# Optimization experiments

Hardware: AMD Instinct MI355X
Metric: run time of the kernel (lower is better)

The kernel has to match this reference:

```python
import jax, jax.numpy as jnp
import numpy as np

N, F, B = 16384, 1024, 512


def setup_inputs() -> dict:
    key = jax.random.key(0)
    k1, k2, k3, k4, k5 = jax.random.split(key, 5)
    s = 1.0 / np.sqrt(F + B)
    return {
        "behavior": jax.random.normal(k1, (N, B), dtype=jnp.float32),
        "h_prev": jax.random.normal(k2, (N, F), dtype=jnp.float32),
        "c_prev": jax.random.normal(k3, (N, F), dtype=jnp.float32),
        "Wh": jax.random.normal(k4, (4 * F, F), dtype=jnp.float32) * s,
        "Wx": jax.random.normal(k5, (4 * F, B), dtype=jnp.float32) * s,
        "b": jnp.zeros((4 * F,), dtype=jnp.float32),
    }


def reference(behavior, h_prev, c_prev, Wh, Wx, b):
    # Fused single GEMM for all 4 gates: [n, 4F]
    gates = jnp.einsum("nf,gf->ng", h_prev, Wh) + jnp.einsum("nb,gb->ng", behavior, Wx) + b
    i, f, g, o = jnp.split(gates, 4, axis=-1)
    i = jax.nn.sigmoid(i)
    f = jax.nn.sigmoid(f)
    g = jnp.tanh(g)
    o = jax.nn.sigmoid(o)
    c = f * c_prev + i * g
    h = o * jnp.tanh(c)
    return h
```

## Files before the change

kernel.cpp:

```cpp
#include <hip/hip_runtime.h>
#include <hip/hip_bf16.h>
#include <stdint.h>

#define N_ROWS 16384
#define F_DIM  1024
#define B_DIM  512
#define K_DIM  1536
#define G_DIM  4096
#define CB_STR 36

typedef __bf16 v8bf __attribute__((ext_vector_type(8)));
typedef float  v4f  __attribute__((ext_vector_type(4)));

typedef const void __attribute__((address_space(1)))* gptr1;
typedef void       __attribute__((address_space(3)))* lptr3;

__device__ __forceinline__ unsigned short f2bf(float x) {
    union { float f; unsigned int u; } c; c.f = x;
    unsigned int u = c.u;
    return (unsigned short)((u + 0x7FFFu + ((u >> 16) & 1u)) >> 16);
}

__global__ void pack_x(const float* __restrict__ behavior,
                       const float* __restrict__ h_prev,
                       unsigned short* __restrict__ A) {
    const int row = blockIdx.x;
    const int col = threadIdx.x * 8;
    const float* src = (col < F_DIM)
        ? h_prev   + (long)row * F_DIM + col
        : behavior + (long)row * B_DIM + (col - F_DIM);
    float4 lo = *(const float4*)src;
    float4 hi = *(const float4*)(src + 4);
    union { unsigned short u[8]; int4 v; } p;
    p.u[0] = f2bf(lo.x); p.u[1] = f2bf(lo.y); p.u[2] = f2bf(lo.z); p.u[3] = f2bf(lo.w);
    p.u[4] = f2bf(hi.x); p.u[5] = f2bf(hi.y); p.u[6] = f2bf(hi.z); p.u[7] = f2bf(hi.w);
    *(int4*)(A + (long)row * K_DIM + col) = p.v;
}

__global__ void pack_w(const float* __restrict__ Wh,
                       const float* __restrict__ Wx,
                       const float* __restrict__ b,
                       unsigned short* __restrict__ W,
                       float* __restrict__ bperm) {
    const int gp   = blockIdx.x;
    const int gate = gp & 3;
    const int f    = gp >> 2;
    const int g    = gate * F_DIM + f;
    const int col  = threadIdx.x * 8;
    const float* src = (col < F_DIM)
        ? Wh + (long)g * F_DIM + col
        : Wx + (long)g * B_DIM + (col - F_DIM);
    float4 lo = *(const float4*)src;
    float4 hi = *(const float4*)(src + 4);
    union { unsigned short u[8]; int4 v; } p;
    p.u[0] = f2bf(lo.x); p.u[1] = f2bf(lo.y); p.u[2] = f2bf(lo.z); p.u[3] = f2bf(lo.w);
    p.u[4] = f2bf(hi.x); p.u[5] = f2bf(hi.y); p.u[6] = f2bf(hi.z); p.u[7] = f2bf(hi.w);
    *(int4*)(W + (long)gp * K_DIM + col) = p.v;
    if (threadIdx.x == 0) bperm[gp] = b[g];
}

__device__ __forceinline__ float sigmoidf_fast(float x) {
    return 1.f / (1.f + __expf(-x));
}
__device__ __forceinline__ float tanhf_fast(float x) {
    return 1.f - 2.f / (__expf(2.f * x) + 1.f);
}

__global__ __launch_bounds__(256, 2) void lstm_gemm(
    const unsigned short* __restrict__ A,
    const unsigned short* __restrict__ W,
    const float* __restrict__ bperm,
    const float* __restrict__ c_prev,
    float* __restrict__ out)
{
    __shared__ unsigned short lds[16384];

    const int m0   = blockIdx.y * 128;
    const int n0   = blockIdx.x * 128;
    const int tid  = threadIdx.x;
    const int lane = tid & 63;
    const int wave = tid >> 6;
    const int wm   = (wave >> 1) * 64;
    const int wn   = (wave & 1) * 64;
    const int lrow = lane & 15;
    const int quad = lane >> 4;
    const int r7   = lrow & 7;

    v4f acc[4][4] = {};

    const int ls_row = lane >> 3;
    const int ls_blk = (lane & 7) ^ ls_row;
    const unsigned short* a_g = A + (long)(m0 + wave * 32 + ls_row) * K_DIM + ls_blk * 8;
    const unsigned short* w_g = W + (long)(n0 + wave * 32 + ls_row) * K_DIM + ls_blk * 8;
    unsigned short* a_l = &lds[(wave * 32) * 64];
    unsigned short* w_l = &lds[8192 + (wave * 32) * 64];

    for (int k0 = 0; k0 < K_DIM; k0 += 64) {
#pragma unroll
        for (int c = 0; c < 4; ++c) {
            __builtin_amdgcn_global_load_lds((gptr1)(a_g + (long)c * 8 * K_DIM + k0),
                                             (lptr3)(a_l + c * 8 * 64), 16, 0, 0);
            __builtin_amdgcn_global_load_lds((gptr1)(w_g + (long)c * 8 * K_DIM + k0),
                                             (lptr3)(w_l + c * 8 * 64), 16, 0, 0);
        }
        __syncthreads();

#pragma unroll
        for (int kk = 0; kk < 64; kk += 32) {
            const int ko = kk >> 3;
            const int sa = (((quad + ko) ^ r7) * 8);
            v8bf af[4], bf[4];
#pragma unroll
            for (int mt = 0; mt < 4; ++mt)
                af[mt] = *(const v8bf*)&lds[(wm + mt * 16 + lrow) * 64 + sa];
#pragma unroll
            for (int nt = 0; nt < 4; ++nt)
                bf[nt] = *(const v8bf*)&lds[8192 + (wn + nt * 16 + lrow) * 64 + sa];
#pragma unroll
            for (int mt = 0; mt < 4; ++mt)
#pragma unroll
                for (int nt = 0; nt < 4; ++nt)
                    acc[mt][nt] = __builtin_amdgcn_mfma_f32_16x16x32_bf16(
                        af[mt], bf[nt], acc[mt][nt], 0, 0, 0);
        }
        __syncthreads();
    }

    float* cbuf = (float*)lds;
    const int fbase = n0 >> 2;
#pragma unroll
    for (int i = 0; i < 4; ++i) {
        const int q  = i * 256 + tid;
        const int r  = q >> 3;
        const int c4 = (q & 7) * 4;
        *(float4*)&cbuf[r * CB_STR + c4] =
            *(const float4*)&c_prev[(long)(m0 + r) * F_DIM + fbase + c4];
    }
    __syncthreads();

    const int l3 = lane & 3;
    const int fl = (lane & 15) >> 2;
#pragma unroll
    for (int nt = 0; nt < 4; ++nt) {
        const int   gcol = n0 + wn + nt * 16 + lrow;
        const float bias = bperm[gcol];
#pragma unroll
        for (int mt = 0; mt < 4; ++mt) {
            float a0 = acc[mt][nt][0] + bias;
            float a1 = acc[mt][nt][1] + bias;
            float a2 = acc[mt][nt][2] + bias;
            float a3 = acc[mt][nt][3] + bias;
            float s0 = (lane & 1) ? a0 : a1;
            float s1 = (lane & 1) ? a2 : a3;
            float r0 = __shfl_xor(s0, 1, 64);
            float r1 = __shfl_xor(s1, 1, 64);
            if (lane & 1) { a0 = r0; a2 = r1; } else { a1 = r0; a3 = r1; }
            s0 = (lane & 2) ? a0 : a2;
            s1 = (lane & 2) ? a1 : a3;
            r0 = __shfl_xor(s0, 2, 64);
            r1 = __shfl_xor(s1, 2, 64);
            if (lane & 2) { a0 = r0; a1 = r1; } else { a2 = r0; a3 = r1; }
            const float iv = sigmoidf_fast(a0);
            const float fv = sigmoidf_fast(a1);
            const float gv = tanhf_fast(a2);
            const float ov = sigmoidf_fast(a3);
            const int lr = wm + mt * 16 + quad * 4 + l3;
            const int lc = ((wn + nt * 16) >> 2) + fl;
            const float cp = cbuf[lr * CB_STR + lc];
            const float cv = fv * cp + iv * gv;
            cbuf[lr * CB_STR + lc] = ov * tanhf_fast(cv);
        }
    }
    __syncthreads();

#pragma unroll
    for (int i = 0; i < 4; ++i) {
        const int q  = i * 256 + tid;
        const int r  = q >> 3;
        const int c4 = (q & 7) * 4;
        *(float4*)&out[(long)(m0 + r) * F_DIM + fbase + c4] =
            *(const float4*)&cbuf[r * CB_STR + c4];
    }
}

extern "C" void kernel_launch(void* const* d_in, const int* in_sizes, int n_in,
                              void* d_out, int out_size, void* d_ws, size_t ws_size,
                              hipStream_t stream) {
    const float* behavior = (const float*)d_in[0];
    const float* h_prev   = (const float*)d_in[1];
    const float* c_prev   = (const float*)d_in[2];
    const float* Wh       = (const float*)d_in[3];
    const float* Wx       = (const float*)d_in[4];
    const float* b        = (const float*)d_in[5];
    float* out = (float*)d_out;

    unsigned short* A  = (unsigned short*)d_ws;
    unsigned short* W  = A + (size_t)N_ROWS * K_DIM;
    float*       bperm = (float*)(W + (size_t)G_DIM * K_DIM);

    pack_x<<<N_ROWS, 192, 0, stream>>>(behavior, h_prev, A);
    pack_w<<<G_DIM, 192, 0, stream>>>(Wh, Wx, b, W, bperm);
    lstm_gemm<<<dim3(G_DIM / 128, N_ROWS / 128), 256, 0, stream>>>(A, W, bperm, c_prev, out);
}
```

Baseline: 401.4 us.

## Rewrite LSTM GEMM with 256x256 tiles, double-buffered LDS pipeline, and fused packing

Merges the two packing kernels into one launch. Rewrites the GEMM to use 256x256 output tiles with 512 threads and 128KB of dynamic LDS. Global-to-LDS prefetch of the next K tile is double-buffered and overlapped with MFMA work, using explicit waitcnt, barriers and setprio. Block indices are remapped for cache locality. The larger tiles raise data reuse and hide load latency, at the cost of higher LDS and register pressure and lower occupancy.

New measurement: 437.0 us. 1.09x slower.

```diff
diff --git a/kernel.cpp b/kernel.cpp
--- a/kernel.cpp
+++ b/kernel.cpp
@@ -1,13 +1,15 @@
 #include <hip/hip_runtime.h>
 #include <hip/hip_bf16.h>
 #include <stdint.h>
+#include <type_traits>
 
 #define N_ROWS 16384
 #define F_DIM  1024
 #define B_DIM  512
 #define K_DIM  1536
 #define G_DIM  4096
-#define CB_STR 36
+#define NT     24
+#define CB_STR 68
 
 typedef __bf16 v8bf __attribute__((ext_vector_type(8)));
 typedef float  v4f  __attribute__((ext_vector_type(4)));
@@ -21,151 +23,215 @@
     return (unsigned short)((u + 0x7FFFu + ((u >> 16) & 1u)) >> 16);
 }
 
-__global__ void pack_x(const float* __restrict__ behavior,
-                       const float* __restrict__ h_prev,
-                       unsigned short* __restrict__ A) {
-    const int row = blockIdx.x;
+__device__ __forceinline__ float sigmoidf_fast(float x) {
+    return 1.f / (1.f + __expf(-x));
+}
+__device__ __forceinline__ float tanhf_fast(float x) {
+    return 1.f - 2.f / (__expf(2.f * x) + 1.f);
+}
+
+__global__ void pack_all(const float* __restrict__ behavior,
+                         const float* __restrict__ h_prev,
+                         const float* __restrict__ Wh,
+                         const float* __restrict__ Wx,
+                         const float* __restrict__ b,
+                         unsigned short* __restrict__ A,
+                         unsigned short* __restrict__ W,
+                         float* __restrict__ bperm) {
+    const int blk = blockIdx.x;
     const int col = threadIdx.x * 8;
-    const float* src = (col < F_DIM)
-        ? h_prev   + (long)row * F_DIM + col
-        : behavior + (long)row * B_DIM + (col - F_DIM);
+    const float* src;
+    unsigned short* dst;
+    if (blk < N_ROWS) {
+        src = (col < F_DIM) ? h_prev + (long)blk * F_DIM + col
+                            : behavior + (long)blk * B_DIM + (col - F_DIM);
+        dst = A + (long)blk * K_DIM + col;
+    } else {
+        const int gp   = blk - N_ROWS;
+        const int gate = gp & 3;
+        const int f    = gp >> 2;
+        const int g    = gate * F_DIM + f;
+        src = (col < F_DIM) ? Wh + (long)g * F_DIM + col
+                            : Wx + (long)g * B_DIM + (col - F_DIM);
+        dst = W + (long)gp * K_DIM + col;
+        if (threadIdx.x == 0) bperm[gp] = b[g];
+    }
     float4 lo = *(const float4*)src;
     float4 hi = *(const float4*)(src + 4);
     union { unsigned short u[8]; int4 v; } p;
     p.u[0] = f2bf(lo.x); p.u[1] = f2bf(lo.y); p.u[2] = f2bf(lo.z); p.u[3] = f2bf(lo.w);
     p.u[4] = f2bf(hi.x); p.u[5] = f2bf(hi.y); p.u[6] = f2bf(hi.z); p.u[7] = f2bf(hi.w);
-    *(int4*)(A + (long)row * K_DIM + col) = p.v;
-}
-
-__global__ void pack_w(const float* __restrict__ Wh,
-                       const float* __restrict__ Wx,
-                       const float* __restrict__ b,
-                       unsigned short* __restrict__ W,
-                       float* __restrict__ bperm) {
-    const int gp   = blockIdx.x;
-    const int gate = gp & 3;
-    const int f    = gp >> 2;
-    const int g    = gate * F_DIM + f;
-    const int col  = threadIdx.x * 8;
-    const float* src = (col < F_DIM)
-        ? Wh + (long)g * F_DIM + col
-        : Wx + (long)g * B_DIM + (col - F_DIM);
-    float4 lo = *(const float4*)src;
-    float4 hi = *(const float4*)(src + 4);
-    union { unsigned short u[8]; int4 v; } p;
-    p.u[0] = f2bf(lo.x); p.u[1] = f2bf(lo.y); p.u[2] = f2bf(lo.z); p.u[3] = f2bf(lo.w);
-    p.u[4] = f2bf(hi.x); p.u[5] = f2bf(hi.y); p.u[6] = f2bf(hi.z); p.u[7] = f2bf(hi.w);
-    *(int4*)(W + (long)gp * K_DIM + col) = p.v;
-    if (threadIdx.x == 0) bperm[gp] = b[g];
-}
-
-__device__ __forceinline__ float sigmoidf_fast(float x) {
-    return 1.f / (1.f + __expf(-x));
-}
-__device__ __forceinline__ float tanhf_fast(float x) {
-    return 1.f - 2.f / (__expf(2.f * x) + 1.f);
-}
-
-__global__ __launch_bounds__(256, 2) void lstm_gemm(
+    *(int4*)dst = p.v;
+}
+
+__global__ __launch_bounds__(512, 2) void lstm_gemm(
     const unsigned short* __restrict__ A,
     const unsigned short* __restrict__ W,
     const float* __restrict__ bperm,
     const float* __restrict__ c_prev,
     float* __restrict__ out)
 {
-    __shared__ unsigned short lds[16384];
-
-    const int m0   = blockIdx.y * 128;
-    const int n0   = blockIdx.x * 128;
+    extern __shared__ char smem[];
+
+    const int bid = blockIdx.x;
+    const int s   = (bid & 7) * 128 + (bid >> 3);
+    const int m0  = (s & 63) << 8;
+    const int n0  = (s >> 6) << 8;
+
     const int tid  = threadIdx.x;
     const int lane = tid & 63;
     const int wave = tid >> 6;
-    const int wm   = (wave >> 1) * 64;
-    const int wn   = (wave & 1) * 64;
+    const int wmi  = wave >> 2;
+    const int wni  = wave & 3;
     const int lrow = lane & 15;
     const int quad = lane >> 4;
-    const int r7   = lrow & 7;
-
-    v4f acc[4][4] = {};
-
-    const int ls_row = lane >> 3;
-    const int ls_blk = (lane & 7) ^ ls_row;
-    const unsigned short* a_g = A + (long)(m0 + wave * 32 + ls_row) * K_DIM + ls_blk * 8;
-    const unsigned short* w_g = W + (long)(n0 + wave * 32 + ls_row) * K_DIM + ls_blk * 8;
-    unsigned short* a_l = &lds[(wave * 32) * 64];
-    unsigned short* w_l = &lds[8192 + (wave * 32) * 64];
-
-    for (int k0 = 0; k0 < K_DIM; k0 += 64) {
-#pragma unroll
-        for (int c = 0; c < 4; ++c) {
-            __builtin_amdgcn_global_load_lds((gptr1)(a_g + (long)c * 8 * K_DIM + k0),
-                                             (lptr3)(a_l + c * 8 * 64), 16, 0, 0);
-            __builtin_amdgcn_global_load_lds((gptr1)(w_g + (long)c * 8 * K_DIM + k0),
-                                             (lptr3)(w_l + c * 8 * 64), 16, 0, 0);
+
+    const int ar   = wmi * 128 + lrow;
+    const int aoff = ar * 64 + ((quad ^ (ar & 3)) << 4);
+    const int br   = wni * 64 + lrow;
+    const int boff = br * 64 + ((quad ^ (br & 3)) << 4);
+
+    const int r0 = tid >> 2,         d0 = tid & 3;
+    const int r1 = (tid + 512) >> 2, d1 = tid & 3;
+    const unsigned short* aS0 = A + (long)(m0 + r0) * K_DIM + ((d0 ^ (r0 & 3)) << 3);
+    const unsigned short* aS1 = A + (long)(m0 + r1) * K_DIM + ((d1 ^ (r1 & 3)) << 3);
+    const unsigned short* wS0 = W + (long)(n0 + r0) * K_DIM + ((d0 ^ (r0 & 3)) << 3);
+    const unsigned short* wS1 = W + (long)(n0 + r1) * K_DIM + ((d1 ^ (r1 & 3)) << 3);
+    const int du0 = wave * 1024;
+    const int du1 = du0 + 8192;
+
+    v4f acc[8][4] = {};
+
+    auto stageA = [&](int plane, int koff) {
+        __builtin_amdgcn_global_load_lds((gptr1)(aS0 + koff),
+                                         (lptr3)(smem + (plane << 14) + du0), 16, 0, 0);
+        __builtin_amdgcn_global_load_lds((gptr1)(aS1 + koff),
+                                         (lptr3)(smem + (plane << 14) + du1), 16, 0, 0);
+    };
+    auto stageB = [&](int plane, int koff) {
+        __builtin_amdgcn_global_load_lds((gptr1)(wS0 + koff),
+                                         (lptr3)(smem + 65536 + (plane << 14) + du0), 16, 0, 0);
+        __builtin_amdgcn_global_load_lds((gptr1)(wS1 + koff),
+                                         (lptr3)(smem + 65536 + (plane << 14) + du1), 16, 0, 0);
+    };
+
+#define MFMA_BLK(MB)                                                            \
+    __builtin_amdgcn_s_setprio(1);                                              \
+    _Pragma("unroll")                                                           \
+    for (int mt = 0; mt < 4; ++mt)                                              \
+        _Pragma("unroll")                                                       \
+        for (int nt = 0; nt < 4; ++nt)                                          \
+            acc[(MB)*4 + mt][nt] = __builtin_amdgcn_mfma_f32_16x16x32_bf16(     \
+                afr[mt], bfr[nt], acc[(MB)*4 + mt][nt], 0, 0, 0);               \
+    __builtin_amdgcn_s_setprio(0);
+
+    auto tile = [&](int BUF, int kn, auto pf_tag) {
+        constexpr bool PF = decltype(pf_tag)::value;
+        const char* A0p = smem + ((BUF * 2 + 0) << 14);
+        const char* A1p = smem + ((BUF * 2 + 1) << 14);
+        const char* B0p = A0p + 65536;
+        const char* B1p = A1p + 65536;
+        const int   pb  = (BUF ^ 1) * 2;
+        v8bf afr[4], bfr[4];
+
+#pragma unroll
+        for (int nt = 0; nt < 4; ++nt) bfr[nt] = *(const v8bf*)(B0p + nt * 1024 + boff);
+#pragma unroll
+        for (int mt = 0; mt < 4; ++mt) afr[mt] = *(const v8bf*)(A0p + mt * 1024 + aoff);
+        if constexpr (PF) stageA(pb + 0, kn);
+        __builtin_amdgcn_s_barrier();
+        asm volatile("s_waitcnt lgkmcnt(0)" ::: "memory");
+        MFMA_BLK(0)
+        __builtin_amdgcn_s_barrier();
+
+#pragma unroll
+        for (int mt = 0; mt < 4; ++mt) afr[mt] = *(const v8bf*)(A0p + (4 + mt) * 1024 + aoff);
+        if constexpr (PF) {
+            stageB(pb + 0, kn);
+            asm volatile("s_waitcnt vmcnt(4)" ::: "memory");
+        } else {
+            asm volatile("s_waitcnt vmcnt(0)" ::: "memory");
         }
-        __syncthreads();
-
-#pragma unroll
-        for (int kk = 0; kk < 64; kk += 32) {
-            const int ko = kk >> 3;
-            const int sa = (((quad + ko) ^ r7) * 8);
-            v8bf af[4], bf[4];
-#pragma unroll
-            for (int mt = 0; mt < 4; ++mt)
-                af[mt] = *(const v8bf*)&lds[(wm + mt * 16 + lrow) * 64 + sa];
-#pragma unroll
-            for (int nt = 0; nt < 4; ++nt)
-                bf[nt] = *(const v8bf*)&lds[8192 + (wn + nt * 16 + lrow) * 64 + sa];
-#pragma unroll
-            for (int mt = 0; mt < 4; ++mt)
-#pragma unroll
-                for (int nt = 0; nt < 4; ++nt)
-                    acc[mt][nt] = __builtin_amdgcn_mfma_f32_16x16x32_bf16(
-                        af[mt], bf[nt], acc[mt][nt], 0, 0, 0);
+        __builtin_amdgcn_s_barrier();
+        asm volatile("s_waitcnt lgkmcnt(0)" ::: "memory");
+        MFMA_BLK(1)
+        __builtin_amdgcn_s_barrier();
+
+#pragma unroll
+        for (int nt = 0; nt < 4; ++nt) bfr[nt] = *(const v8bf*)(B1p + nt * 1024 + boff);
+#pragma unroll
+        for (int mt = 0; mt < 4; ++mt) afr[mt] = *(const v8bf*)(A1p + mt * 1024 + aoff);
+        if constexpr (PF) stageA(pb + 1, kn + 32);
+        __builtin_amdgcn_s_barrier();
+        asm volatile("s_waitcnt lgkmcnt(0)" ::: "memory");
+        MFMA_BLK(0)
+        __builtin_amdgcn_s_barrier();
+
+#pragma unroll
+        for (int mt = 0; mt < 4; ++mt) afr[mt] = *(const v8bf*)(A1p + (4 + mt) * 1024 + aoff);
+        if constexpr (PF) {
+            stageB(pb + 1, kn + 32);
+            asm volatile("s_waitcnt vmcnt(4)" ::: "memory");
         }
-        __syncthreads();
-    }
-
-    float* cbuf = (float*)lds;
+        __builtin_amdgcn_s_barrier();
+        asm volatile("s_waitcnt lgkmcnt(0)" ::: "memory");
+        MFMA_BLK(1)
+        __builtin_amdgcn_s_barrier();
+    };
+
+    stageA(0, 0);  stageB(0, 0);
+    stageA(1, 32); stageB(1, 32);
+    asm volatile("s_waitcnt vmcnt(4)" ::: "memory");
+    __builtin_amdgcn_s_barrier();
+
+    int kn = 64;
+    for (int t = 0; t < NT - 1; ++t) {
+        tile(t & 1, kn, std::true_type{});
+        kn += 64;
+    }
+    tile((NT - 1) & 1, 0, std::false_type{});
+#undef MFMA_BLK
+
+    float* cbuf = (float*)smem;
     const int fbase = n0 >> 2;
 #pragma unroll
-    for (int i = 0; i < 4; ++i) {
-        const int q  = i * 256 + tid;
-        const int r  = q >> 3;
-        const int c4 = (q & 7) * 4;
+    for (int i = 0; i < 8; ++i) {
+        const int q  = i * 512 + tid;
+        const int r  = q >> 4;
+        const int c4 = (q & 15) << 2;
         *(float4*)&cbuf[r * CB_STR + c4] =
             *(const float4*)&c_prev[(long)(m0 + r) * F_DIM + fbase + c4];
     }
     __syncthreads();
 
     const int l3 = lane & 3;
-    const int fl = (lane & 15) >> 2;
+    const int fl = (lane >> 2) & 3;
 #pragma unroll
     for (int nt = 0; nt < 4; ++nt) {
-        const int   gcol = n0 + wn + nt * 16 + lrow;
+        const int   gcol = n0 + wni * 64 + nt * 16 + lrow;
         const float bias = bperm[gcol];
 #pragma unroll
-        for (int mt = 0; mt < 4; ++mt) {
+        for (int mt = 0; mt < 8; ++mt) {
             float a0 = acc[mt][nt][0] + bias;
             float a1 = acc[mt][nt][1] + bias;
             float a2 = acc[mt][nt][2] + bias;
             float a3 = acc[mt][nt][3] + bias;
             float s0 = (lane & 1) ? a0 : a1;
             float s1 = (lane & 1) ? a2 : a3;
-            float r0 = __shfl_xor(s0, 1, 64);
-            float r1 = __shfl_xor(s1, 1, 64);
-            if (lane & 1) { a0 = r0; a2 = r1; } else { a1 = r0; a3 = r1; }
+            float t0 = __shfl_xor(s0, 1, 64);
+            float t1 = __shfl_xor(s1, 1, 64);
+            if (lane & 1) { a0 = t0; a2 = t1; } else { a1 = t0; a3 = t1; }
             s0 = (lane & 2) ? a0 : a2;
             s1 = (lane & 2) ? a1 : a3;
-            r0 = __shfl_xor(s0, 2, 64);
-            r1 = __shfl_xor(s1, 2, 64);
-            if (lane & 2) { a0 = r0; a1 = r1; } else { a2 = r0; a3 = r1; }
+            t0 = __shfl_xor(s0, 2, 64);
+            t1 = __shfl_xor(s1, 2, 64);
+            if (lane & 2) { a0 = t0; a1 = t1; } else { a2 = t0; a3 = t1; }
             const float iv = sigmoidf_fast(a0);
             const float fv = sigmoidf_fast(a1);
             const float gv = tanhf_fast(a2);
             const float ov = sigmoidf_fast(a3);
-            const int lr = wm + mt * 16 + quad * 4 + l3;
-            const int lc = ((wn + nt * 16) >> 2) + fl;
+            const int lr = wmi * 128 + mt * 16 + quad * 4 + l3;
+            const int lc = wni * 16 + nt * 4 + fl;
             const float cp = cbuf[lr * CB_STR + lc];
             const float cv = fv * cp + iv * gv;
             cbuf[lr * CB_STR + lc] = ov * tanhf_fast(cv);
@@ -174,10 +240,10 @@
     __syncthreads();
 
 #pragma unroll
-    for (int i = 0; i < 4; ++i) {
-        const int q  = i * 256 + tid;
-        const int r  = q >> 3;
-        const int c4 = (q & 7) * 4;
+    for (int i = 0; i < 8; ++i) {
+        const int q  = i * 512 + tid;
+        const int r  = q >> 4;
+        const int c4 = (q & 15) << 2;
         *(float4*)&out[(long)(m0 + r) * F_DIM + fbase + c4] =
             *(const float4*)&cbuf[r * CB_STR + c4];
     }
@@ -198,7 +264,9 @@
     unsigned short* W  = A + (size_t)N_ROWS * K_DIM;
     float*       bperm = (float*)(W + (size_t)G_DIM * K_DIM);
 
-    pack_x<<<N_ROWS, 192, 0, stream>>>(behavior, h_prev, A);
-    pack_w<<<G_DIM, 192, 0, stream>>>(Wh, Wx, b, W, bperm);
-    lstm_gemm<<<dim3(G_DIM / 128, N_ROWS / 128), 256, 0, stream>>>(A, W, bperm, c_prev, out);
-}
+    hipFuncSetAttribute(reinterpret_cast<const void*>(lstm_gemm),
+                        hipFuncAttributeMaxDynamicSharedMemorySize, 131072);
+
+    pack_all<<<N_ROWS + G_DIM, 192, 0, stream>>>(behavior, h_prev, Wh, Wx, b, A, W, bperm);
+    lstm_gemm<<<dim3((N_ROWS / 256) * (G_DIM / 256)), 512, 131072, stream>>>(A, W, bperm, c_prev, out);
+}
```
